# Kernel tuning notes

Hardware: AMD Instinct MI355X
Metric: run time of the kernel (lower is better)

Reference implementation:

```python
import jax, jax.numpy as jnp
import numpy as np

B, S, N, D = 1, 512, 384, 64
H, DP, DQK = 32, 128, 64
LAMBDA_INIT = 1.0
EPS = 1e-32
SCALING = DQK ** -0.5


def _layer_norm(x, g, b):
    m = jnp.mean(x, axis=-1, keepdims=True)
    v = jnp.mean(jnp.square(x - m), axis=-1, keepdims=True)
    return (x - m) * jax.lax.rsqrt(v + 1e-5) * g + b


def setup_inputs() -> dict:
    key = jax.random.key(0)
    ks = jax.random.split(key, 12)
    msa = jax.random.normal(ks[0], (B, S, N, D), dtype=jnp.float32)
    Wq = jax.random.normal(ks[1], (2 * DQK, D), dtype=jnp.float32) * 0.02
    Wk = Wq + jax.random.normal(ks[2], (2 * DQK, D), dtype=jnp.float32) * 0.1 * 0.02
    Wl = jax.random.normal(ks[3], (H, D), dtype=jnp.float32) * 0.02
    Wr = jax.random.normal(ks[4], (H, D), dtype=jnp.float32) * 0.02
    Wp = jax.random.normal(ks[5], (2 * DP, H * H), dtype=jnp.float32) * 0.02
    bp = jnp.zeros((2 * DP,), dtype=jnp.float32)
    lq1 = jax.random.normal(ks[6], (DQK,), dtype=jnp.float32) * 0.1
    lk1 = jax.random.normal(ks[7], (DQK,), dtype=jnp.float32) * 0.1
    lq2 = jax.random.normal(ks[8], (DQK,), dtype=jnp.float32) * 0.1
    lk2 = jax.random.normal(ks[9], (DQK,), dtype=jnp.float32) * 0.1
    return {
        'msa': msa,
        'ln_g': jnp.ones((D,), jnp.float32), 'ln_b': jnp.zeros((D,), jnp.float32),
        'Wq': Wq, 'Wk': Wk,
        'qn_g': jnp.ones((DQK,), jnp.float32), 'qn_b': jnp.zeros((DQK,), jnp.float32),
        'kn_g': jnp.ones((DQK,), jnp.float32), 'kn_b': jnp.zeros((DQK,), jnp.float32),
        'lq1': lq1, 'lk1': lk1, 'lq2': lq2, 'lk2': lk2,
        'Wl': Wl, 'Wr': Wr, 'Wp': Wp, 'bp': bp,
    }


def reference(msa, ln_g, ln_b, Wq, Wk, qn_g, qn_b, kn_g, kn_b,
              lq1, lk1, lq2, lk2, Wl, Wr, Wp, bp):
    b, s, n, d = msa.shape
    x = _layer_norm(msa, ln_g, ln_b)  # [b,s,n,d]

    # differential sequence attention (all masks are all-True by default)
    q = (x[:, 0] @ Wq.T).reshape(b, n, 2, DQK).transpose(0, 2, 1, 3)       # [b,2,n,dqk]
    k = (x @ Wk.T).reshape(b, s, n, 2, DQK).transpose(0, 3, 1, 2, 4)       # [b,2,s,n,dqk]
    q = _layer_norm(q, qn_g, qn_b)
    k = _layer_norm(k, kn_g, kn_b)
    sw = jnp.einsum('btnd,btsnd->btsn', q, k) * SCALING                     # [b,2,s,n]
    sw = sw.sum(axis=-1) / (n + EPS)                                        # [b,2,s]
    lam = jnp.exp(jnp.sum(lq1 * lk1)) - jnp.exp(jnp.sum(lq2 * lk2)) + LAMBDA_INIT
    sw = sw[:, 0] - lam * sw[:, 1]                                          # [b,s]
    seq_weights = jax.nn.softmax(sw, axis=-1)                               # [b,s]

    # weighted left/right hidden projections
    a = jnp.einsum('bsnd,hd->bnsh', x, Wl)
    bt = jnp.einsum('bsnd,hd->bnsh', x, Wr)
    ws = jnp.sqrt(seq_weights + EPS)[:, None, :, None]                      # [b,1,s,1]
    a = a * ws
    bt = bt * ws

    # outer product mean over sequences, then pairwise projection + SwiGLU
    outer = jnp.einsum('bisc,bjse->bijce', a, bt).reshape(b, n, n, H * H)   # [b,n,n,h^2]
    out = outer @ Wp.T + bp                                                 # [b,n,n,2*dp]
    val, gate = jnp.split(out, 2, axis=-1)
    return jax.nn.silu(gate) * val                                          # [b,n,n,dp]
```

## Files before the change

### kernel.cpp

```cpp
#include <hip/hip_runtime.h>
#include <hip/hip_bf16.h>
#include <math.h>

#define WS_X        0u
#define WS_AEXT     12582912u
#define WS_BEXT     18874368u
#define WS_QG       25165824u
#define WS_SQG      25214976u
#define WS_SQB      25215744u
#define WS_PART     25216512u
#define WS_WSQ      25219584u
#define WS_BPP      25220096u
#define WS_WPF      25220352u

typedef __attribute__((ext_vector_type(8))) short bf16x8;
typedef __attribute__((ext_vector_type(4))) float f32x4;

union U4B8 { uint4 u4; unsigned u[4]; bf16x8 v; };

__device__ __forceinline__ unsigned short f2b(float x) {
    __hip_bfloat16 b = __float2bfloat16(x);
    return *reinterpret_cast<unsigned short*>(&b);
}
__device__ __forceinline__ float b2f(unsigned short u) {
    __hip_bfloat16 b = *reinterpret_cast<__hip_bfloat16*>(&u);
    return __bfloat162float(b);
}

#define GLDS(g, l) __builtin_amdgcn_global_load_lds(                                   \
    (const __attribute__((address_space(1))) unsigned int*)(g),                        \
    (__attribute__((address_space(3))) unsigned int*)(l), 16, 0, 0)

__global__ __launch_bounds__(256) void k1_ln(const float* __restrict__ msa,
                                             const float* __restrict__ g,
                                             const float* __restrict__ bb,
                                             float* __restrict__ x) {
    int row = blockIdx.x * 16 + (threadIdx.x >> 4);
    int l16 = threadIdx.x & 15;
    float4 v = ((const float4*)msa)[(size_t)row * 16 + l16];
    float sum = v.x + v.y + v.z + v.w;
    #pragma unroll
    for (int m = 1; m < 16; m <<= 1) sum += __shfl_xor(sum, m);
    float mean = sum * (1.0f / 64.0f);
    float4 dv = make_float4(v.x - mean, v.y - mean, v.z - mean, v.w - mean);
    float sq = dv.x * dv.x + dv.y * dv.y + dv.z * dv.z + dv.w * dv.w;
    #pragma unroll
    for (int m = 1; m < 16; m <<= 1) sq += __shfl_xor(sq, m);
    float r = rsqrtf(sq * (1.0f / 64.0f) + 1e-5f);
    float4 g4 = ((const float4*)g)[l16];
    float4 b4 = ((const float4*)bb)[l16];
    ((float4*)x)[(size_t)row * 16 + l16] = make_float4(
        dv.x * r * g4.x + b4.x, dv.y * r * g4.y + b4.y,
        dv.z * r * g4.z + b4.z, dv.w * r * g4.w + b4.w);
}

__global__ __launch_bounds__(128) void k2_q(const float* __restrict__ x,
                                            const float* __restrict__ Wq,
                                            const float* __restrict__ qg_,
                                            const float* __restrict__ qb_,
                                            const float* __restrict__ kg_,
                                            const float* __restrict__ kb_,
                                            float* __restrict__ qgOut,
                                            float* __restrict__ SqgOut,
                                            float* __restrict__ SqbOut) {
    int n = blockIdx.x;
    int tt = threadIdx.x >> 6;
    int d = threadIdx.x & 63;
    const float* xr = x + (size_t)n * 64;
    const float* w  = Wq + (size_t)(tt * 64 + d) * 64;
    float acc = 0.f;
    #pragma unroll 8
    for (int dd = 0; dd < 64; ++dd) acc += xr[dd] * w[dd];
    float sum = acc;
    #pragma unroll
    for (int m = 1; m < 64; m <<= 1) sum += __shfl_xor(sum, m);
    float mean = sum * (1.0f / 64.0f);
    float dv = acc - mean;
    float sq = dv * dv;
    #pragma unroll
    for (int m = 1; m < 64; m <<= 1) sq += __shfl_xor(sq, m);
    float r = rsqrtf(sq * (1.0f / 64.0f) + 1e-5f);
    float qnv = dv * r * qg_[d] + qb_[d];
    float qgv = qnv * kg_[d];
    float sb  = qnv * kb_[d];
    float sg  = qgv;
    #pragma unroll
    for (int m = 1; m < 64; m <<= 1) { sg += __shfl_xor(sg, m); sb += __shfl_xor(sb, m); }
    qgOut[(size_t)(tt * 384 + n) * 64 + d] = qgv;
    if (d == 0) { SqgOut[tt * 384 + n] = sg; SqbOut[tt * 384 + n] = sb; }
}

__global__ __launch_bounds__(256) void gemm_k3(const float* __restrict__ X,
                                               const float* __restrict__ Wk,
                                               const float* __restrict__ qg,
                                               const float* __restrict__ Sqg,
                                               const float* __restrict__ Sqb,
                                               float* __restrict__ part) {
    __shared__ __align__(16) char smem[65536];
    float (*AsT)[132] = (float(*)[132])smem;
    float (*BsT)[132] = (float(*)[132])(smem + 16896);
    float* kbuf = (float*)smem;

    int t  = threadIdx.x;
    int m0 = blockIdx.x * 128;
    int s  = m0 / 384;
    int nchunk = (m0 - s * 384) >> 7;
    int tr = t >> 4, tc = t & 15;
    float acc[8][8] = {};
    int rrow = t >> 3;
    int kk   = (t & 7) * 4;
    for (int k0 = 0; k0 < 64; k0 += 32) {
        #pragma unroll
        for (int l = 0; l < 4; ++l) {
            int row = rrow + 32 * l;
            float4 va = *(const float4*)(X + (size_t)(m0 + row) * 64 + k0 + kk);
            AsT[kk + 0][row] = va.x; AsT[kk + 1][row] = va.y;
            AsT[kk + 2][row] = va.z; AsT[kk + 3][row] = va.w;
            float4 vb = *(const float4*)(Wk + (size_t)row * 64 + k0 + kk);
            BsT[kk + 0][row] = vb.x; BsT[kk + 1][row] = vb.y;
            BsT[kk + 2][row] = vb.z; BsT[kk + 3][row] = vb.w;
        }
        __syncthreads();
        #pragma unroll 4
        for (int k = 0; k < 32; ++k) {
            float a[8], b[8];
            *(float4*)&a[0] = *(const float4*)&AsT[k][tr * 8];
            *(float4*)&a[4] = *(const float4*)&AsT[k][tr * 8 + 4];
            *(float4*)&b[0] = *(const float4*)&BsT[k][tc * 8];
            *(float4*)&b[4] = *(const float4*)&BsT[k][tc * 8 + 4];
            #pragma unroll
            for (int q = 0; q < 8; ++q)
                #pragma unroll
                for (int j = 0; j < 8; ++j)
                    acc[q][j] += a[q] * b[j];
        }
        __syncthreads();
    }
    #pragma unroll
    for (int q = 0; q < 8; ++q) {
        int m = tr * 8 + q;
        int swz = (m & 15) << 4;
        int b0 = m * 512 + (((tc * 2) * 16) ^ swz);
        int b1 = m * 512 + (((tc * 2 + 1) * 16) ^ swz);
        *(float4*)((char*)kbuf + b0) = make_float4(acc[q][0], acc[q][1], acc[q][2], acc[q][3]);
        *(float4*)((char*)kbuf + b1) = make_float4(acc[q][4], acc[q][5], acc[q][6], acc[q][7]);
    }
    __syncthreads();
    int r  = t & 127;
    int tt = t >> 7;
    int n  = nchunk * 128 + r;
    const char* base = (const char*)kbuf + r * 512;
    const float4* qgp = (const float4*)(qg + ((size_t)(tt * 384 + n)) * 64);
    int swz = (r & 15) << 4;
    float s1 = 0.f, s2 = 0.f, s3 = 0.f;
    #pragma unroll
    for (int i = 0; i < 16; ++i) {
        float4 kv = *(const float4*)(base + ((((tt * 16 + i) * 16) ^ swz)));
        float4 qv = qgp[i];
        s1 += kv.x + kv.y + kv.z + kv.w;
        s2 += kv.x * kv.x + kv.y * kv.y + kv.z * kv.z + kv.w * kv.w;
        s3 += kv.x * qv.x + kv.y * qv.y + kv.z * qv.z + kv.w * qv.w;
    }
    float mu  = s1 * (1.0f / 64.0f);
    float var = s2 * (1.0f / 64.0f) - mu * mu;
    float rln = rsqrtf(var + 1e-5f);
    float dot = rln * (s3 - mu * Sqg[tt * 384 + n]) + Sqb[tt * 384 + n];
    #pragma unroll
    for (int m = 1; m < 64; m <<= 1) dot += __shfl_xor(dot, m);
    __syncthreads();
    if ((t & 63) == 0) kbuf[t >> 6] = dot;
    __syncthreads();
    if (t == 0) part[((size_t)0 * 512 + s) * 3 + nchunk] = kbuf[0] + kbuf[1];
    if (t == 1) part[((size_t)1 * 512 + s) * 3 + nchunk] = kbuf[2] + kbuf[3];
}

__global__ __launch_bounds__(512) void k4_softmax(const float* __restrict__ part,
                                                  const float* __restrict__ lq1,
                                                  const float* __restrict__ lk1,
                                                  const float* __restrict__ lq2,
                                                  const float* __restrict__ lk2,
                                                  float* __restrict__ wsq) {
    int s = threadIdx.x;
    float l1 = 0.f, l2 = 0.f;
    for (int i = 0; i < 64; ++i) { l1 += lq1[i] * lk1[i]; l2 += lq2[i] * lk2[i]; }
    float lam = expf(l1) - expf(l2) + 1.0f;
    const float c = 0.125f / 384.0f;
    float a0 = (part[s * 3] + part[s * 3 + 1] + part[s * 3 + 2]) * c;
    float a1 = (part[(512 + s) * 3] + part[(512 + s) * 3 + 1] + part[(512 + s) * 3 + 2]) * c;
    float v = a0 - lam * a1;
    __shared__ float red[512];
    red[s] = v;
    __syncthreads();
    for (int off = 256; off > 0; off >>= 1) {
        if (s < off) red[s] = fmaxf(red[s], red[s + off]);
        __syncthreads();
    }
    float mx = red[0];
    __syncthreads();
    float e = expf(v - mx);
    red[s] = e;
    __syncthreads();
    for (int off = 256; off > 0; off >>= 1) {
        if (s < off) red[s] += red[s + off];
        __syncthreads();
    }
    wsq[s] = sqrtf(e / red[0] + 1e-32f);
}

__global__ __launch_bounds__(256) void k5_ab(const float* __restrict__ x,
                                             const float* __restrict__ Wl,
                                             const float* __restrict__ Wr,
                                             const float* __restrict__ wsq,
                                             unsigned short* __restrict__ AHo,
                                             unsigned short* __restrict__ ALo,
                                             unsigned short* __restrict__ BHo,
                                             unsigned short* __restrict__ BLo) {
    int i  = blockIdx.x;
    int s0 = blockIdx.y * 64;
    int t  = threadIdx.x;
    __shared__ __align__(16) float wl[2048], wr[2048];
    __shared__ float xT[64][69];
    ((float4*)wl)[t * 2]     = ((const float4*)Wl)[t * 2];
    ((float4*)wl)[t * 2 + 1] = ((const float4*)Wl)[t * 2 + 1];
    ((float4*)wr)[t * 2]     = ((const float4*)Wr)[t * 2];
    ((float4*)wr)[t * 2 + 1] = ((const float4*)Wr)[t * 2 + 1];
    {
        int s_l = t >> 2, d0 = (t & 3) * 16;
        const float* xr = x + ((size_t)(s0 + s_l) * 384 + i) * 64 + d0;
        #pragma unroll
        for (int j = 0; j < 4; ++j) {
            float4 v = *(const float4*)(xr + j * 4);
            xT[d0 + j * 4 + 0][s_l] = v.x; xT[d0 + j * 4 + 1][s_l] = v.y;
            xT[d0 + j * 4 + 2][s_l] = v.z; xT[d0 + j * 4 + 3][s_l] = v.w;
        }
    }
    __syncthreads();
    int c = t >> 3, so = (t & 7) * 8;
    float aa[8] = {}, bb2[8] = {};
    #pragma unroll 8
    for (int d = 0; d < 64; ++d) {
        float wlv = wl[c * 64 + d], wrv = wr[c * 64 + d];
        #pragma unroll
        for (int q = 0; q < 8; ++q) {
            float xv = xT[d][so + q];
            aa[q]  += xv * wlv;
            bb2[q] += xv * wrv;
        }
    }
    #pragma unroll
    for (int q = 0; q < 8; ++q) {
        float wq = wsq[s0 + so + q];
        aa[q] *= wq; bb2[q] *= wq;
    }
    int m = i * 32 + c;
    int s = s0 + so;
    size_t idx = (((size_t)(m >> 4) * 16 + (s >> 5)) * 64 + ((m & 15) | (((s >> 3) & 3) << 4))) * 8;
    {
        unsigned short h[8], l[8];
        #pragma unroll
        for (int q = 0; q < 8; ++q) { h[q] = f2b(aa[q]); l[q] = f2b(aa[q] - b2f(h[q])); }
        *(uint4*)&AHo[idx] = make_uint4((unsigned)h[0] | ((unsigned)h[1] << 16), (unsigned)h[2] | ((unsigned)h[3] << 16),
                                        (unsigned)h[4] | ((unsigned)h[5] << 16), (unsigned)h[6] | ((unsigned)h[7] << 16));
        *(uint4*)&ALo[idx] = make_uint4((unsigned)l[0] | ((unsigned)l[1] << 16), (unsigned)l[2] | ((unsigned)l[3] << 16),
                                        (unsigned)l[4] | ((unsigned)l[5] << 16), (unsigned)l[6] | ((unsigned)l[7] << 16));
    }
    {
        unsigned short h[8], l[8];
        #pragma unroll
        for (int q = 0; q < 8; ++q) { h[q] = f2b(bb2[q]); l[q] = f2b(bb2[q] - b2f(h[q])); }
        *(uint4*)&BHo[idx] = make_uint4((unsigned)h[0] | ((unsigned)h[1] << 16), (unsigned)h[2] | ((unsigned)h[3] << 16),
                                        (unsigned)h[4] | ((unsigned)h[5] << 16), (unsigned)h[6] | ((unsigned)h[7] << 16));
        *(uint4*)&BLo[idx] = make_uint4((unsigned)l[0] | ((unsigned)l[1] << 16), (unsigned)l[2] | ((unsigned)l[3] << 16),
                                        (unsigned)l[4] | ((unsigned)l[5] << 16), (unsigned)l[6] | ((unsigned)l[7] << 16));
    }
}

__global__ __launch_bounds__(256) void prep_wp(const float* __restrict__ Wp,
                                               const float* __restrict__ bp,
                                               unsigned short* __restrict__ WpF,
                                               float* __restrict__ bpP) {
    int gid = blockIdx.x * 256 + threadIdx.x;
    int lane  = gid & 63;
    int kstep = (gid >> 6) & 31;
    int nb    = (gid >> 11) & 15;
    int bsel  = gid >> 15;
    int rl = lane & 15, kg = lane >> 4;
    int urow = nb * 16 + rl;
    int srow = (urow & 1) ? 128 + (urow >> 1) : (urow >> 1);
    int k0 = kstep * 32 + kg * 8;
    const float* src = Wp + (size_t)srow * 1024 + k0;
    unsigned short o[8];
    #pragma unroll
    for (int e = 0; e < 8; ++e) {
        float w = src[e];
        unsigned short h = f2b(w);
        o[e] = bsel ? f2b(w - b2f(h)) : h;
    }
    *(uint4*)&WpF[(size_t)gid * 8] = make_uint4(
        (unsigned)o[0] | ((unsigned)o[1] << 16), (unsigned)o[2] | ((unsigned)o[3] << 16),
        (unsigned)o[4] | ((unsigned)o[5] << 16), (unsigned)o[6] | ((unsigned)o[7] << 16));
    if (blockIdx.x == 0) {
        int tt = threadIdx.x;
        bpP[tt] = bp[(tt & 1) ? 128 + (tt >> 1) : (tt >> 1)];
    }
}

__global__ __launch_bounds__(512, 2) void gemm_fused(const unsigned short* __restrict__ AH,
                                                     const unsigned short* __restrict__ AL,
                                                     const unsigned short* __restrict__ BHm,
                                                     const unsigned short* __restrict__ BLm,
                                                     const unsigned short* __restrict__ WpF,
                                                     const float* __restrict__ bpP,
                                                     float* __restrict__ out) {
    __shared__ __align__(16) unsigned char smem[131072];
    unsigned* pa = (unsigned*)smem;

    const int t = threadIdx.x;
    const int wave = t >> 6, lane = t & 63;
    const int bx = blockIdx.x, by = blockIdx.y;
    const int m0 = bx * 256, n0 = by * 256;
    const int wr = wave & 3;
    const int wc = wave >> 2;
    const int kgrp = lane >> 4, rl = lane & 15;
    f32x4 acc[4][8] = {};

    const unsigned short* srcArr = (wave < 2) ? AH : (wave < 4) ? AL : (wave < 6) ? BHm : BLm;
    const int pbase = (((wave < 4) ? m0 : n0) >> 4) + (wave & 1) * 8;
    const unsigned short* srcBase = srcArr + (size_t)pbase * 8192 + lane * 8;
    unsigned short* dstW = (unsigned short*)smem + (wave >> 1) * 8192 + (wave & 1) * 4096;

    #pragma unroll
    for (int p = 0; p < 8; ++p)
        GLDS(srcBase + (size_t)p * 8192, dstW + p * 512);

    for (int kt = 0; kt < 16; ++kt) {
        if (kt < 15) {
            unsigned short* dst = dstW + ((kt + 1) & 1) * 32768;
            const unsigned short* s2 = srcBase + (size_t)(kt + 1) * 512;
            #pragma unroll
            for (int p = 0; p < 8; ++p)
                GLDS(s2 + (size_t)p * 8192, dst + p * 512);
            asm volatile("s_waitcnt vmcnt(8)" ::: "memory");
        } else {
            asm volatile("s_waitcnt vmcnt(0)" ::: "memory");
        }
        __builtin_amdgcn_s_barrier();
        asm volatile("" ::: "memory");
        const int cb = (kt & 1) * 65536;
        bf16x8 aHf[4], aLf[4];
        #pragma unroll
        for (int mf = 0; mf < 4; ++mf) {
            const int pA = (wr * 4 + mf) * 1024;
            aHf[mf] = *(const bf16x8*)(smem + cb + pA + lane * 16);
            aLf[mf] = *(const bf16x8*)(smem + cb + 16384 + pA + lane * 16);
        }
        __builtin_amdgcn_s_setprio(1);
        #pragma unroll
        for (int nf = 0; nf < 8; ++nf) {
            const int pB = (wc * 8 + nf) * 1024;
            bf16x8 bHf = *(const bf16x8*)(smem + cb + 32768 + pB + lane * 16);
            bf16x8 bLf = *(const bf16x8*)(smem + cb + 49152 + pB + lane * 16);
            #pragma unroll
            for (int mf = 0; mf < 4; ++mf) {
                acc[mf][nf] = __builtin_amdgcn_mfma_f32_16x16x32_bf16(aHf[mf], bHf, acc[mf][nf], 0, 0, 0);
                acc[mf][nf] = __builtin_amdgcn_mfma_f32_16x16x32_bf16(aLf[mf], bHf, acc[mf][nf], 0, 0, 0);
                acc[mf][nf] = __builtin_amdgcn_mfma_f32_16x16x32_bf16(aHf[mf], bLf, acc[mf][nf], 0, 0, 0);
            }
        }
        __builtin_amdgcn_s_setprio(0);
        asm volatile("" ::: "memory");
        __builtin_amdgcn_s_barrier();
        asm volatile("" ::: "memory");
    }

    for (int g = 0; g < 4; ++g) {
        if (wr == g) {
            #pragma unroll
            for (int mf = 0; mf < 4; ++mf)
                #pragma unroll
                for (int nf = 0; nf < 8; ++nf) {
                    int pl = ((mf >> 1) << 3) + wc * 4 + (nf >> 1);
                    #pragma unroll
                    for (int r = 0; r < 4; ++r) {
                        int k = (((mf & 1) * 16 + kgrp * 4 + r) << 5) | ((nf & 1) * 16 + rl);
                        float v = acc[mf][nf][r];
                        unsigned short h = f2b(v);
                        unsigned short l = f2b(v - b2f(h));
                        pa[(pl << 10) + (k ^ ((pl & 3) << 3))] = (unsigned)h | ((unsigned)l << 16);
                    }
                }
        }
        __syncthreads();

        f32x4 acc2[2] = {};
        const unsigned* paRow = pa + (rl << 10);
        const int kg8 = kgrp * 8;
        #pragma unroll 4
        for (int ks = 0; ks < 32; ++ks) {
            U4B8 ua0, ua1, aHf, aLf;
            int kb = (ks * 32 + kg8) ^ ((rl & 3) << 3);
            ua0.u4 = *(const uint4*)(paRow + kb);
            ua1.u4 = *(const uint4*)(paRow + kb + 4);
            aHf.u[0] = __builtin_amdgcn_perm(ua0.u[1], ua0.u[0], 0x05040100u);
            aHf.u[1] = __builtin_amdgcn_perm(ua0.u[3], ua0.u[2], 0x05040100u);
            aHf.u[2] = __builtin_amdgcn_perm(ua1.u[1], ua1.u[0], 0x05040100u);
            aHf.u[3] = __builtin_amdgcn_perm(ua1.u[3], ua1.u[2], 0x05040100u);
            aLf.u[0] = __builtin_amdgcn_perm(ua0.u[1], ua0.u[0], 0x07060302u);
            aLf.u[1] = __builtin_amdgcn_perm(ua0.u[3], ua0.u[2], 0x07060302u);
            aLf.u[2] = __builtin_amdgcn_perm(ua1.u[1], ua1.u[0], 0x07060302u);
            aLf.u[3] = __builtin_amdgcn_perm(ua1.u[3], ua1.u[2], 0x07060302u);
            #pragma unroll
            for (int nf2 = 0; nf2 < 2; ++nf2) {
                const int nb = wave * 2 + nf2;
                bf16x8 bHf = *(const bf16x8*)&WpF[(size_t)((nb * 32 + ks) * 64 + lane) * 8];
                bf16x8 bLf = *(const bf16x8*)&WpF[(size_t)(((16 + nb) * 32 + ks) * 64 + lane) * 8];
                acc2[nf2] = __builtin_amdgcn_mfma_f32_16x16x32_bf16(aHf.v, bHf, acc2[nf2], 0, 0, 0);
                acc2[nf2] = __builtin_amdgcn_mfma_f32_16x16x32_bf16(aLf.v, bHf, acc2[nf2], 0, 0, 0);
                acc2[nf2] = __builtin_amdgcn_mfma_f32_16x16x32_bf16(aHf.v, bLf, acc2[nf2], 0, 0, 0);
            }
        }

        const int parity = rl & 1;
        #pragma unroll
        for (int nf2 = 0; nf2 < 2; ++nf2) {
            const int np = wave * 32 + nf2 * 16 + rl;
            const float bias = bpP[np];
            const int ocol = np >> 1;
            #pragma unroll
            for (int r = 0; r < 4; ++r) {
                float own = acc2[nf2][r] + bias;
                float oth = __shfl_xor(own, 1);
                float v = parity ? oth : own;
                float gg = parity ? own : oth;
                float res = v * (gg / (1.0f + expf(-gg)));
                if (parity == (r >> 1)) {
                    int pl2 = kgrp * 4 + r;
                    int i = bx * 8 + g * 2 + (pl2 >> 3);
                    int j = by * 8 + (pl2 & 7);
                    out[((size_t)i * 384 + j) * 128 + ocol] = res;
                }
            }
        }
        __syncthreads();
    }
}

extern "C" void kernel_launch(void* const* d_in, const int* in_sizes, int n_in,
                              void* d_out, int out_size, void* d_ws, size_t ws_size,
                              hipStream_t stream) {
    const float* msa  = (const float*)d_in[0];
    const float* ln_g = (const float*)d_in[1];
    const float* ln_b = (const float*)d_in[2];
    const float* Wq   = (const float*)d_in[3];
    const float* Wk   = (const float*)d_in[4];
    const float* qn_g = (const float*)d_in[5];
    const float* qn_b = (const float*)d_in[6];
    const float* kn_g = (const float*)d_in[7];
    const float* kn_b = (const float*)d_in[8];
    const float* lq1  = (const float*)d_in[9];
    const float* lk1  = (const float*)d_in[10];
    const float* lq2  = (const float*)d_in[11];
    const float* lk2  = (const float*)d_in[12];
    const float* Wl   = (const float*)d_in[13];
    const float* Wr   = (const float*)d_in[14];
    const float* Wp   = (const float*)d_in[15];
    const float* bp   = (const float*)d_in[16];
    float* out = (float*)d_out;
    float* ws  = (float*)d_ws;

    float* x = ws + WS_X;
    unsigned short* AHs = (unsigned short*)(ws + WS_AEXT);
    unsigned short* ALs = (unsigned short*)(ws + WS_AEXT + 3145728u);
    unsigned short* BHs = (unsigned short*)(ws + WS_BEXT);
    unsigned short* BLs = (unsigned short*)(ws + WS_BEXT + 3145728u);
    float* qg   = ws + WS_QG;
    float* Sqg  = ws + WS_SQG;
    float* Sqb  = ws + WS_SQB;
    float* part = ws + WS_PART;
    float* wsq  = ws + WS_WSQ;
    float* bpP  = ws + WS_BPP;
    unsigned short* WpF = (unsigned short*)(ws + WS_WPF);

    prep_wp<<<256, 256, 0, stream>>>(Wp, bp, WpF, bpP);
    k1_ln<<<12288, 256, 0, stream>>>(msa, ln_g, ln_b, x);
    k2_q<<<384, 128, 0, stream>>>(x, Wq, qn_g, qn_b, kn_g, kn_b, qg, Sqg, Sqb);
    gemm_k3<<<1536, 256, 0, stream>>>(x, Wk, qg, Sqg, Sqb, part);
    k4_softmax<<<1, 512, 0, stream>>>(part, lq1, lk1, lq2, lk2, wsq);
    k5_ab<<<dim3(384, 8), 256, 0, stream>>>(x, Wl, Wr, wsq, AHs, ALs, BHs, BLs);
    gemm_fused<<<dim3(48, 48), 512, 0, stream>>>(AHs, ALs, BHs, BLs, WpF, bpP, out);
}
```

Measured before the change: 932.8 us.

## Load A fragments directly to registers and double-buffer epilogue spill

The main GEMM loop stops staging the A operand through LDS and loads the A hi/lo fragments straight from global memory into double-buffered registers. Only B is staged in LDS, with a two-step-ahead prefetch and finer-grained barriers interleaved with the MFMA groups. The epilogue now alternates two LDS buffers so the next wave group's accumulator spill overlaps the current group's second GEMM, dropping one __syncthreads per group. The cost is more register pressure from the A register buffers, more barriers per k-step, and uncoalesced-looking direct global loads of A.

```diff
diff --git a/kernel.cpp b/kernel.cpp
--- a/kernel.cpp
+++ b/kernel.cpp
@@ -30,6 +30,8 @@
 #define GLDS(g, l) __builtin_amdgcn_global_load_lds(                                   \
     (const __attribute__((address_space(1))) unsigned int*)(g),                        \
     (__attribute__((address_space(3))) unsigned int*)(l), 16, 0, 0)
+
+#define MFMA16(a, b, c) __builtin_amdgcn_mfma_f32_16x16x32_bf16((a), (b), (c), 0, 0, 0)
 
 __global__ __launch_bounds__(256) void k1_ln(const float* __restrict__ msa,
                                              const float* __restrict__ g,
@@ -313,7 +315,6 @@
                                                      const float* __restrict__ bpP,
                                                      float* __restrict__ out) {
     __shared__ __align__(16) unsigned char smem[131072];
-    unsigned* pa = (unsigned*)smem;
 
     const int t = threadIdx.x;
     const int wave = t >> 6, lane = t & 63;
@@ -324,76 +325,105 @@
     const int kgrp = lane >> 4, rl = lane & 15;
     f32x4 acc[4][8] = {};
 
-    const unsigned short* srcArr = (wave < 2) ? AH : (wave < 4) ? AL : (wave < 6) ? BHm : BLm;
-    const int pbase = (((wave < 4) ? m0 : n0) >> 4) + (wave & 1) * 8;
-    const unsigned short* srcBase = srcArr + (size_t)pbase * 8192 + lane * 8;
-    unsigned short* dstW = (unsigned short*)smem + (wave >> 1) * 8192 + (wave & 1) * 4096;
-
-    #pragma unroll
-    for (int p = 0; p < 8; ++p)
-        GLDS(srcBase + (size_t)p * 8192, dstW + p * 512);
-
+    const unsigned short* aHb = AH + (size_t)((m0 + wr * 64) >> 4) * 8192 + lane * 8;
+    const unsigned short* aLb = AL + (size_t)((m0 + wr * 64) >> 4) * 8192 + lane * 8;
+    const int half = wave & 1, qtr = wave >> 1;
+    const unsigned short* bSrc = (half ? BLm : BHm) + (size_t)((n0 >> 4) + qtr * 4) * 8192 + lane * 8;
+    unsigned short* smem_s = (unsigned short*)smem;
+    unsigned short* bDst = smem_s + half * 8192 + qtr * 2048;
+
+    bf16x8 aHr[2][4], aLr[2][4];
+    #pragma unroll
+    for (int p = 0; p < 4; ++p) {
+        GLDS(bSrc + (size_t)p * 8192,       bDst + p * 512);
+        GLDS(bSrc + (size_t)p * 8192 + 512, bDst + 16384 + p * 512);
+    }
+    #pragma unroll
+    for (int f = 0; f < 4; ++f) {
+        aHr[0][f] = *(const bf16x8*)(aHb + (size_t)f * 8192);
+        aLr[0][f] = *(const bf16x8*)(aLb + (size_t)f * 8192);
+    }
+    __syncthreads();
+
+    #pragma unroll 2
     for (int kt = 0; kt < 16; ++kt) {
-        if (kt < 15) {
-            unsigned short* dst = dstW + ((kt + 1) & 1) * 32768;
-            const unsigned short* s2 = srcBase + (size_t)(kt + 1) * 512;
+        const int cur = kt & 1, nxt = cur ^ 1;
+        const int cb = cur * 32768;
+        #pragma unroll
+        for (int p = 0; p < 4; ++p) {
+            bf16x8 bHf[2], bLf[2];
             #pragma unroll
-            for (int p = 0; p < 8; ++p)
-                GLDS(s2 + (size_t)p * 8192, dst + p * 512);
-            asm volatile("s_waitcnt vmcnt(8)" ::: "memory");
-        } else {
-            asm volatile("s_waitcnt vmcnt(0)" ::: "memory");
-        }
-        __builtin_amdgcn_s_barrier();
-        asm volatile("" ::: "memory");
-        const int cb = (kt & 1) * 65536;
-        bf16x8 aHf[4], aLf[4];
-        #pragma unroll
-        for (int mf = 0; mf < 4; ++mf) {
-            const int pA = (wr * 4 + mf) * 1024;
-            aHf[mf] = *(const bf16x8*)(smem + cb + pA + lane * 16);
-            aLf[mf] = *(const bf16x8*)(smem + cb + 16384 + pA + lane * 16);
-        }
-        __builtin_amdgcn_s_setprio(1);
-        #pragma unroll
-        for (int nf = 0; nf < 8; ++nf) {
-            const int pB = (wc * 8 + nf) * 1024;
-            bf16x8 bHf = *(const bf16x8*)(smem + cb + 32768 + pB + lane * 16);
-            bf16x8 bLf = *(const bf16x8*)(smem + cb + 49152 + pB + lane * 16);
+            for (int q = 0; q < 2; ++q) {
+                const int nf = p * 2 + q;
+                const int pB = (wc * 8 + nf) * 1024;
+                bHf[q] = *(const bf16x8*)(smem + cb + pB + lane * 16);
+                bLf[q] = *(const bf16x8*)(smem + cb + 16384 + pB + lane * 16);
+            }
+            asm volatile("" ::: "memory");
+            __builtin_amdgcn_s_barrier();
+            asm volatile("" ::: "memory");
+            __builtin_amdgcn_s_setprio(1);
             #pragma unroll
-            for (int mf = 0; mf < 4; ++mf) {
-                acc[mf][nf] = __builtin_amdgcn_mfma_f32_16x16x32_bf16(aHf[mf], bHf, acc[mf][nf], 0, 0, 0);
-                acc[mf][nf] = __builtin_amdgcn_mfma_f32_16x16x32_bf16(aLf[mf], bHf, acc[mf][nf], 0, 0, 0);
-                acc[mf][nf] = __builtin_amdgcn_mfma_f32_16x16x32_bf16(aHf[mf], bLf, acc[mf][nf], 0, 0, 0);
+            for (int q = 0; q < 2; ++q) {
+                const int nf = p * 2 + q;
+                #pragma unroll
+                for (int mf = 0; mf < 4; ++mf) {
+                    acc[mf][nf] = MFMA16(aHr[cur][mf], bHf[q], acc[mf][nf]);
+                    acc[mf][nf] = MFMA16(aLr[cur][mf], bHf[q], acc[mf][nf]);
+                    acc[mf][nf] = MFMA16(aHr[cur][mf], bLf[q], acc[mf][nf]);
+                }
             }
-        }
-        __builtin_amdgcn_s_setprio(0);
-        asm volatile("" ::: "memory");
-        __builtin_amdgcn_s_barrier();
-        asm volatile("" ::: "memory");
-    }
-
-    for (int g = 0; g < 4; ++g) {
-        if (wr == g) {
-            #pragma unroll
-            for (int mf = 0; mf < 4; ++mf)
-                #pragma unroll
-                for (int nf = 0; nf < 8; ++nf) {
-                    int pl = ((mf >> 1) << 3) + wc * 4 + (nf >> 1);
+            __builtin_amdgcn_s_setprio(0);
+            if (p == 3) {
+                if (kt < 14) {
+                    const unsigned short* s2 = bSrc + (size_t)(kt + 2) * 512;
                     #pragma unroll
-                    for (int r = 0; r < 4; ++r) {
-                        int k = (((mf & 1) * 16 + kgrp * 4 + r) << 5) | ((nf & 1) * 16 + rl);
-                        float v = acc[mf][nf][r];
-                        unsigned short h = f2b(v);
-                        unsigned short l = f2b(v - b2f(h));
-                        pa[(pl << 10) + (k ^ ((pl & 3) << 3))] = (unsigned)h | ((unsigned)l << 16);
+                    for (int pp = 0; pp < 4; ++pp)
+                        GLDS(s2 + (size_t)pp * 8192, bDst + cur * 16384 + pp * 512);
+                    asm volatile("s_waitcnt vmcnt(12)" ::: "memory");
+                } else {
+                    asm volatile("s_waitcnt vmcnt(8)" ::: "memory");
+                }
+                if (kt < 15) {
+                    #pragma unroll
+                    for (int f = 0; f < 4; ++f) {
+                        aHr[nxt][f] = *(const bf16x8*)(aHb + (size_t)f * 8192 + (size_t)(kt + 1) * 512);
+                        aLr[nxt][f] = *(const bf16x8*)(aLb + (size_t)f * 8192 + (size_t)(kt + 1) * 512);
                     }
                 }
-        }
-        __syncthreads();
+            }
+            asm volatile("" ::: "memory");
+            __builtin_amdgcn_s_barrier();
+            asm volatile("" ::: "memory");
+        }
+    }
+
+    auto SPILL = [&](unsigned* pa) {
+        #pragma unroll
+        for (int mf = 0; mf < 4; ++mf)
+            #pragma unroll
+            for (int nf = 0; nf < 8; ++nf) {
+                int pl = ((mf >> 1) << 3) + wc * 4 + (nf >> 1);
+                #pragma unroll
+                for (int r = 0; r < 4; ++r) {
+                    int k = (((mf & 1) * 16 + kgrp * 4 + r) << 5) | ((nf & 1) * 16 + rl);
+                    float v = acc[mf][nf][r];
+                    unsigned short h = f2b(v);
+                    unsigned short l = f2b(v - b2f(h));
+                    pa[(pl << 10) + (k ^ ((pl & 3) << 3))] = (unsigned)h | ((unsigned)l << 16);
+                }
+            }
+    };
+
+    if (wr == 0) SPILL((unsigned*)smem);
+    __syncthreads();
+
+    for (int g = 0; g < 4; ++g) {
+        if (g < 3 && wr == g + 1) SPILL((unsigned*)(smem + (unsigned)((g + 1) & 1) * 65536));
+        const unsigned* paG = (const unsigned*)(smem + (unsigned)(g & 1) * 65536);
 
         f32x4 acc2[2] = {};
-        const unsigned* paRow = pa + (rl << 10);
+        const unsigned* paRow = paG + (rl << 10);
         const int kg8 = kgrp * 8;
         #pragma unroll 4
         for (int ks = 0; ks < 32; ++ks) {
@@ -414,9 +444,9 @@
                 const int nb = wave * 2 + nf2;
                 bf16x8 bHf = *(const bf16x8*)&WpF[(size_t)((nb * 32 + ks) * 64 + lane) * 8];
                 bf16x8 bLf = *(const bf16x8*)&WpF[(size_t)(((16 + nb) * 32 + ks) * 64 + lane) * 8];
-                acc2[nf2] = __builtin_amdgcn_mfma_f32_16x16x32_bf16(aHf.v, bHf, acc2[nf2], 0, 0, 0);
-                acc2[nf2] = __builtin_amdgcn_mfma_f32_16x16x32_bf16(aLf.v, bHf, acc2[nf2], 0, 0, 0);
-                acc2[nf2] = __builtin_amdgcn_mfma_f32_16x16x32_bf16(aHf.v, bLf, acc2[nf2], 0, 0, 0);
+                acc2[nf2] = MFMA16(aHf.v, bHf, acc2[nf2]);
+                acc2[nf2] = MFMA16(aLf.v, bHf, acc2[nf2]);
+                acc2[nf2] = MFMA16(aHf.v, bLf, acc2[nf2]);
             }
         }
 
```

Result: slower. 1.488 ms (+59.5%).
